# Kernel optimization log

Measured on AMD Instinct MI355X. Metric: run time of the kernel, lower is better.

Reference implementation:

```python
import jax, jax.numpy as jnp
import numpy as np

N = 100000
E = 1600000
F_IN = 512
H1, C1 = 8, 8      # layer-1: 8 heads, 8 dims each (concat -> 64)
H2, C2 = 1, 16     # layer-2: 1 head, num_classes=16
SLOPE = 0.2        # GATConv leaky_relu negative slope


def setup_inputs() -> dict:
    key = jax.random.key(0)
    ks = jax.random.split(key, 10)
    x = jax.random.normal(ks[0], (N, F_IN), dtype=jnp.float32)
    edge_index = jax.random.randint(ks[1], (2, E), 0, N, dtype=jnp.int32)
    s = 0.05
    W1 = jax.random.normal(ks[2], (F_IN, H1 * C1), dtype=jnp.float32) * s
    a1_src = jax.random.normal(ks[3], (H1, C1), dtype=jnp.float32) * s
    a1_dst = jax.random.normal(ks[4], (H1, C1), dtype=jnp.float32) * s
    b1 = jnp.zeros((H1 * C1,), dtype=jnp.float32)
    W2 = jax.random.normal(ks[5], (H1 * C1, H2 * C2), dtype=jnp.float32) * s
    a2_src = jax.random.normal(ks[6], (H2, C2), dtype=jnp.float32) * s
    a2_dst = jax.random.normal(ks[7], (H2, C2), dtype=jnp.float32) * s
    b2 = jnp.zeros((H2 * C2,), dtype=jnp.float32)
    return {"x": x, "edge_index": edge_index, "W1": W1, "a1_src": a1_src,
            "a1_dst": a1_dst, "b1": b1, "W2": W2, "a2_src": a2_src,
            "a2_dst": a2_dst, "b2": b2}


def _gat_conv(h, src, dst, W, a_src, a_dst, b, heads, ch):
    n = h.shape[0]
    hp = (h @ W).reshape(n, heads, ch)                      # [N,H,C]
    al_s = jnp.einsum('nhc,hc->nh', hp, a_src)              # [N,H]
    al_d = jnp.einsum('nhc,hc->nh', hp, a_dst)              # [N,H]
    e = jax.nn.leaky_relu(al_s[src] + al_d[dst], SLOPE)     # [E,H]
    # segment softmax over edges sharing a destination (self-loops guarantee >=1 edge/node)
    emax = jax.lax.stop_gradient(jax.ops.segment_max(e, dst, num_segments=n))
    ee = jnp.exp(e - emax[dst])
    denom = jax.ops.segment_sum(ee, dst, num_segments=n)
    alpha = ee / denom[dst]                                 # [E,H]
    msg = hp[src] * alpha[:, :, None]                       # [E,H,C]
    out = jax.ops.segment_sum(msg, dst, num_segments=n)     # [N,H,C]
    return out.reshape(n, heads * ch) + b


def reference(x, edge_index, W1, a1_src, a1_dst, b1, W2, a2_src, a2_dst, b2):
    n = x.shape[0]
    loops = jnp.arange(n, dtype=edge_index.dtype)           # add_self_loops=True
    src = jnp.concatenate([edge_index[0], loops])
    dst = jnp.concatenate([edge_index[1], loops])
    h = jax.nn.elu(_gat_conv(x, src, dst, W1, a1_src, a1_dst, b1, H1, C1))
    h = _gat_conv(h, src, dst, W2, a2_src, a2_dst, b2, H2, C2)
    return jax.nn.log_softmax(h, axis=1)
```

## Files before the change

### kernel.cpp

```cpp
#include <hip/hip_runtime.h>
#include <hip/hip_bf16.h>

#define N_NODES 100000
#define F_IN    512
#define H1      8
#define C1      8
#define D1      64
#define C2      16
#define SLOPE   0.2f
#define CAP     48
#define PSHIFT  9
#define PPART   196
#define CAPP    9216
#define CHUNK   4096

typedef __bf16 bf16_t;
typedef bf16_t bf16x8 __attribute__((ext_vector_type(8)));
typedef float  f32x4  __attribute__((ext_vector_type(4)));

__global__ __launch_bounds__(256) void wcvt_kernel(
    const float* __restrict__ W, bf16_t* __restrict__ Bt)
{
    int i = blockIdx.x * 256 + threadIdx.x;
    if (i >= 64 * 512) return;
    int nn = i >> 9, k = i & 511;
    Bt[i] = (bf16_t)W[k * 64 + nn];
}

__global__ __launch_bounds__(256) void part_kernel(
    const int* __restrict__ ei, int* __restrict__ pcnt, int2* __restrict__ pfifo,
    int E, int total)
{
    __shared__ int hist[PPART];
    __shared__ int lofs[PPART];
    __shared__ int gbase[PPART];
    __shared__ int cursor[PPART];
    __shared__ int sdata[256];
    __shared__ int2 fifo[CHUNK];

    const int t = threadIdx.x;
    const int chunk0 = (int)blockIdx.x * CHUNK;

    for (int i = t; i < PPART; i += 256) hist[i] = 0;
    __syncthreads();

    int srcs[16], dsts[16];
    const int e0 = chunk0 + t * 16;
    if (e0 + 16 <= E) {
#pragma unroll
        for (int q = 0; q < 4; ++q) {
            int4 s = *(const int4*)(ei + e0 + q * 4);
            int4 d = *(const int4*)(ei + E + e0 + q * 4);
            srcs[q*4+0]=s.x; srcs[q*4+1]=s.y; srcs[q*4+2]=s.z; srcs[q*4+3]=s.w;
            dsts[q*4+0]=d.x; dsts[q*4+1]=d.y; dsts[q*4+2]=d.z; dsts[q*4+3]=d.w;
        }
    } else {
#pragma unroll
        for (int j = 0; j < 16; ++j) {
            int e = e0 + j;
            if (e < E)          { srcs[j] = ei[e]; dsts[j] = ei[E + e]; }
            else if (e < total) { srcs[j] = dsts[j] = e - E; }
            else                { srcs[j] = -1;    dsts[j] = -1; }
        }
    }
#pragma unroll
    for (int j = 0; j < 16; ++j)
        if (dsts[j] >= 0) atomicAdd(&hist[dsts[j] >> PSHIFT], 1);
    __syncthreads();

    int hv = (t < PPART) ? hist[t] : 0;
    sdata[t] = hv;
    __syncthreads();
    for (int off = 1; off < 256; off <<= 1) {
        int x = (t >= off) ? sdata[t - off] : 0;
        __syncthreads();
        sdata[t] += x;
        __syncthreads();
    }
    if (t < PPART) {
        int lo = sdata[t] - hv;
        lofs[t]   = lo;
        cursor[t] = lo;
        gbase[t]  = hv ? atomicAdd(&pcnt[t], hv) : 0;
    }
    __syncthreads();

#pragma unroll
    for (int j = 0; j < 16; ++j) {
        if (dsts[j] >= 0) {
            int p = dsts[j] >> PSHIFT;
            int slot = atomicAdd(&cursor[p], 1);
            fifo[slot] = make_int2(srcs[j], dsts[j]);
        }
    }
    __syncthreads();

    const int w = t >> 6, lane = t & 63;
    for (int p = w; p < PPART; p += 4) {
        int len = hist[p];
        int lo  = lofs[p];
        int gb  = gbase[p];
        int2* dstp = pfifo + (size_t)p * CAPP;
        for (int j = lane; j < len; j += 64) {
            int g = gb + j;
            if (g < CAPP) dstp[g] = fifo[lo + j];
        }
    }
}

__global__ __launch_bounds__(256) void place_kernel(
    const int2* __restrict__ pfifo, const int* __restrict__ pcnt,
    int* __restrict__ buckets, int* __restrict__ cnt, int n)
{
    __shared__ int lcnt[1 << PSHIFT];
    const int p = blockIdx.x;
    const int dbase = p << PSHIFT;
    const int nd = min(1 << PSHIFT, n - dbase);
    const int t = threadIdx.x;
    for (int i = t; i < nd; i += 256) lcnt[i] = 0;
    __syncthreads();

    int len = pcnt[p]; if (len > CAPP) len = CAPP;
    const int2* f = pfifo + (size_t)p * CAPP;

    int i = t;
    for (; i + 768 < len; i += 1024) {
        int2 e0 = f[i], e1 = f[i + 256], e2 = f[i + 512], e3 = f[i + 768];
        int s0 = atomicAdd(&lcnt[e0.y - dbase], 1);
        int s1 = atomicAdd(&lcnt[e1.y - dbase], 1);
        int s2 = atomicAdd(&lcnt[e2.y - dbase], 1);
        int s3 = atomicAdd(&lcnt[e3.y - dbase], 1);
        if (s0 < CAP) buckets[(size_t)e0.y * CAP + s0] = e0.x;
        if (s1 < CAP) buckets[(size_t)e1.y * CAP + s1] = e1.x;
        if (s2 < CAP) buckets[(size_t)e2.y * CAP + s2] = e2.x;
        if (s3 < CAP) buckets[(size_t)e3.y * CAP + s3] = e3.x;
    }
    for (; i < len; i += 256) {
        int2 e = f[i];
        int s = atomicAdd(&lcnt[e.y - dbase], 1);
        if (s < CAP) buckets[(size_t)e.y * CAP + s] = e.x;
    }
    __syncthreads();
    for (int i2 = t; i2 < nd; i2 += 256) cnt[dbase + i2] = min(lcnt[i2], CAP);
}

__global__ __launch_bounds__(256) void gemm1_kernel(
    const float* __restrict__ X, const bf16_t* __restrict__ Bt,
    const float* __restrict__ a1s, const float* __restrict__ a1d,
    bf16_t* __restrict__ HPb, float* __restrict__ als1, float* __restrict__ ald1,
    int n)
{
    __shared__ __align__(16) bf16_t Asm[4096];
    __shared__ __align__(16) bf16_t Bsm[4096];

    const int t = threadIdx.x;
    const int rowbase = (int)blockIdx.x * 64;
    const int wave = t >> 6;
    const int lane = t & 63;

    const int srow  = t >> 2;
    const int skloc = (t & 3) * 16;

    const int grow = rowbase + srow;
    const bool rok = grow < n;
    const float*  xrow = X  + (size_t)grow * F_IN;
    const bf16_t* brow = Bt + (size_t)srow * F_IN;

    int offA[2];
#pragma unroll
    for (int u = 0; u < 2; ++u) {
        int kloc = skloc + u * 8;
        int s    = kloc >> 5;
        int quad = (kloc >> 3) & 3;
        offA[u] = s * 2048 + (((srow >> 4) * 64) + quad * 16 + (srow & 15)) * 8;
    }

    f32x4 acc[4];
#pragma unroll
    for (int nt = 0; nt < 4; ++nt) acc[nt] = (f32x4){0.f, 0.f, 0.f, 0.f};

    for (int k0 = 0; k0 < F_IN; k0 += 64) {
        float4 xa0, xa1, xa2, xa3;
        if (rok) {
            xa0 = *(const float4*)(xrow + k0 + skloc + 0);
            xa1 = *(const float4*)(xrow + k0 + skloc + 4);
            xa2 = *(const float4*)(xrow + k0 + skloc + 8);
            xa3 = *(const float4*)(xrow + k0 + skloc + 12);
        } else {
            xa0 = xa1 = xa2 = xa3 = make_float4(0.f, 0.f, 0.f, 0.f);
        }
        bf16x8 bb0 = *(const bf16x8*)(brow + k0 + skloc);
        bf16x8 bb1 = *(const bf16x8*)(brow + k0 + skloc + 8);

        __syncthreads();

        bf16x8 af0, af1;
        af0[0]=(bf16_t)xa0.x; af0[1]=(bf16_t)xa0.y; af0[2]=(bf16_t)xa0.z; af0[3]=(bf16_t)xa0.w;
        af0[4]=(bf16_t)xa1.x; af0[5]=(bf16_t)xa1.y; af0[6]=(bf16_t)xa1.z; af0[7]=(bf16_t)xa1.w;
        af1[0]=(bf16_t)xa2.x; af1[1]=(bf16_t)xa2.y; af1[2]=(bf16_t)xa2.z; af1[3]=(bf16_t)xa2.w;
        af1[4]=(bf16_t)xa3.x; af1[5]=(bf16_t)xa3.y; af1[6]=(bf16_t)xa3.z; af1[7]=(bf16_t)xa3.w;
        *(bf16x8*)(Asm + offA[0]) = af0;
        *(bf16x8*)(Asm + offA[1]) = af1;
        *(bf16x8*)(Bsm + offA[0]) = bb0;
        *(bf16x8*)(Bsm + offA[1]) = bb1;

        __syncthreads();

#pragma unroll
        for (int s = 0; s < 2; ++s) {
            bf16x8 a = *(const bf16x8*)(Asm + s * 2048 + (wave * 64 + lane) * 8);
#pragma unroll
            for (int nt = 0; nt < 4; ++nt) {
                bf16x8 b = *(const bf16x8*)(Bsm + s * 2048 + (nt * 64 + lane) * 8);
                acc[nt] = __builtin_amdgcn_mfma_f32_16x16x32_bf16(a, b, acc[nt], 0, 0, 0);
            }
        }
    }

    const int colg = lane & 15;
    const int quad = lane >> 4;
    const int b    = colg >> 3;
    float cs[4], cd[4];
#pragma unroll
    for (int nt = 0; nt < 4; ++nt) {
        cs[nt] = a1s[nt * 16 + colg];
        cd[nt] = a1d[nt * 16 + colg];
    }

#pragma unroll
    for (int i = 0; i < 4; ++i) {
        int r = rowbase + wave * 16 + quad * 4 + i;
        bool ok = r < n;
        if (ok) {
            bf16_t* hr = HPb + (size_t)r * D1;
            hr[colg]      = (bf16_t)acc[0][i];
            hr[16 + colg] = (bf16_t)acc[1][i];
            hr[32 + colg] = (bf16_t)acc[2][i];
            hr[48 + colg] = (bf16_t)acc[3][i];
        }
#pragma unroll
        for (int nt = 0; nt < 4; ++nt) {
            float ps = acc[nt][i] * cs[nt];
            float pd = acc[nt][i] * cd[nt];
            ps += __shfl_xor(ps, 1, 64);  pd += __shfl_xor(pd, 1, 64);
            ps += __shfl_xor(ps, 2, 64);  pd += __shfl_xor(pd, 2, 64);
            ps += __shfl_xor(ps, 4, 64);  pd += __shfl_xor(pd, 4, 64);
            if (ok && (colg & 7) == 0) {
                als1[(size_t)r * 8 + 2 * nt + b] = ps;
                ald1[(size_t)r * 8 + 2 * nt + b] = pd;
            }
        }
    }
}

__global__ __launch_bounds__(256) void agg1_kernel(
    const bf16_t* __restrict__ hp1,
    const float* __restrict__ als, const float* __restrict__ ald,
    const int* __restrict__ cnt, const int* __restrict__ buckets,
    const float* __restrict__ b1,
    float* __restrict__ h1, int n)
{
    int node = blockIdx.x * 4 + (threadIdx.x >> 6);
    if (node >= n) return;
    int lane = threadIdx.x & 63;
    int h = lane >> 3;

    int m = cnt[node]; if (m > CAP) m = CAP;
    const int* bp = buckets + (size_t)node * CAP;
    float ad = ald[node * 8 + h];
    float den = 0.f, acc = 0.f;

    int i = 0;
    for (; i + 8 <= m; i += 8) {
        int s0 = bp[i + 0], s1 = bp[i + 1], s2 = bp[i + 2], s3 = bp[i + 3];
        int s4 = bp[i + 4], s5 = bp[i + 5], s6 = bp[i + 6], s7 = bp[i + 7];
        float a0 = als[s0 * 8 + h], a1 = als[s1 * 8 + h];
        float a2 = als[s2 * 8 + h], a3 = als[s3 * 8 + h];
        float a4 = als[s4 * 8 + h], a5 = als[s5 * 8 + h];
        float a6 = als[s6 * 8 + h], a7 = als[s7 * 8 + h];
        float v0 = (float)hp1[(size_t)s0 * D1 + lane];
        float v1 = (float)hp1[(size_t)s1 * D1 + lane];
        float v2 = (float)hp1[(size_t)s2 * D1 + lane];
        float v3 = (float)hp1[(size_t)s3 * D1 + lane];
        float v4 = (float)hp1[(size_t)s4 * D1 + lane];
        float v5 = (float)hp1[(size_t)s5 * D1 + lane];
        float v6 = (float)hp1[(size_t)s6 * D1 + lane];
        float v7 = (float)hp1[(size_t)s7 * D1 + lane];
        float e0 = a0 + ad; e0 = (e0 > 0.f) ? e0 : SLOPE * e0;
        float e1 = a1 + ad; e1 = (e1 > 0.f) ? e1 : SLOPE * e1;
        float e2 = a2 + ad; e2 = (e2 > 0.f) ? e2 : SLOPE * e2;
        float e3 = a3 + ad; e3 = (e3 > 0.f) ? e3 : SLOPE * e3;
        float e4 = a4 + ad; e4 = (e4 > 0.f) ? e4 : SLOPE * e4;
        float e5 = a5 + ad; e5 = (e5 > 0.f) ? e5 : SLOPE * e5;
        float e6 = a6 + ad; e6 = (e6 > 0.f) ? e6 : SLOPE * e6;
        float e7 = a7 + ad; e7 = (e7 > 0.f) ? e7 : SLOPE * e7;
        float w0 = __expf(e0), w1 = __expf(e1), w2 = __expf(e2), w3 = __expf(e3);
        float w4 = __expf(e4), w5 = __expf(e5), w6 = __expf(e6), w7 = __expf(e7);
        den += ((w0 + w1) + (w2 + w3)) + ((w4 + w5) + (w6 + w7));
        acc = fmaf(w0, v0, acc);
        acc = fmaf(w1, v1, acc);
        acc = fmaf(w2, v2, acc);
        acc = fmaf(w3, v3, acc);
        acc = fmaf(w4, v4, acc);
        acc = fmaf(w5, v5, acc);
        acc = fmaf(w6, v6, acc);
        acc = fmaf(w7, v7, acc);
    }
    for (; i < m; ++i) {
        int s = bp[i];
        float e = als[s * 8 + h] + ad;
        e = (e > 0.f) ? e : SLOPE * e;
        float ee = __expf(e);
        den += ee;
        acc = fmaf(ee, (float)hp1[(size_t)s * D1 + lane], acc);
    }
    float v = acc / den + b1[lane];
    v = (v > 0.f) ? v : (__expf(v) - 1.f);
    h1[(size_t)node * D1 + lane] = v;
}

__global__ __launch_bounds__(256) void gemm2_kernel(
    const float* __restrict__ H, const float* __restrict__ W2,
    const float* __restrict__ a2s, const float* __restrict__ a2d,
    bf16_t* __restrict__ HP2b, float* __restrict__ als2, float* __restrict__ ald2,
    int n)
{
    __shared__ float Ws[64 * 16];
    int t = threadIdx.x;
    for (int i = t; i < 1024; i += 256) Ws[i] = W2[i];
    __syncthreads();
    int idx = blockIdx.x * 256 + t;
    int node = idx >> 4, c = idx & 15;
    if (node >= n) return;
    const float* hr = H + (size_t)node * D1;
    float acc = 0.f;
#pragma unroll 8
    for (int k = 0; k < 64; ++k) acc = fmaf(hr[k], Ws[k * 16 + c], acc);
    HP2b[idx] = (bf16_t)acc;

    float rs = acc * a2s[c];
    float rd = acc * a2d[c];
    rs += __shfl_xor(rs, 8, 16);  rd += __shfl_xor(rd, 8, 16);
    rs += __shfl_xor(rs, 4, 16);  rd += __shfl_xor(rd, 4, 16);
    rs += __shfl_xor(rs, 2, 16);  rd += __shfl_xor(rd, 2, 16);
    rs += __shfl_xor(rs, 1, 16);  rd += __shfl_xor(rd, 1, 16);
    if (c == 0) { als2[node] = rs; ald2[node] = rd; }
}

__global__ __launch_bounds__(256) void agg2_kernel(
    const bf16_t* __restrict__ hp2,
    const float* __restrict__ als, const float* __restrict__ ald,
    const int* __restrict__ cnt, const int* __restrict__ buckets,
    const float* __restrict__ b2,
    float* __restrict__ out, int n)
{
    int node = blockIdx.x * 16 + (threadIdx.x >> 4);
    if (node >= n) return;
    int c = threadIdx.x & 15;

    int m0c = cnt[node]; if (m0c > CAP) m0c = CAP;
    const int* bp = buckets + (size_t)node * CAP;
    float ad = ald[node];
    float den = 0.f, acc = 0.f;

    int i = 0;
    for (; i + 8 <= m0c; i += 8) {
        int s0 = bp[i + 0], s1 = bp[i + 1], s2 = bp[i + 2], s3 = bp[i + 3];
        int s4 = bp[i + 4], s5 = bp[i + 5], s6 = bp[i + 6], s7 = bp[i + 7];
        float a0 = als[s0], a1 = als[s1], a2 = als[s2], a3 = als[s3];
        float a4 = als[s4], a5 = als[s5], a6 = als[s6], a7 = als[s7];
        float v0 = (float)hp2[(size_t)s0 * 16 + c];
        float v1 = (float)hp2[(size_t)s1 * 16 + c];
        float v2 = (float)hp2[(size_t)s2 * 16 + c];
        float v3 = (float)hp2[(size_t)s3 * 16 + c];
        float v4 = (float)hp2[(size_t)s4 * 16 + c];
        float v5 = (float)hp2[(size_t)s5 * 16 + c];
        float v6 = (float)hp2[(size_t)s6 * 16 + c];
        float v7 = (float)hp2[(size_t)s7 * 16 + c];
        float e0 = a0 + ad; e0 = (e0 > 0.f) ? e0 : SLOPE * e0;
        float e1 = a1 + ad; e1 = (e1 > 0.f) ? e1 : SLOPE * e1;
        float e2 = a2 + ad; e2 = (e2 > 0.f) ? e2 : SLOPE * e2;
        float e3 = a3 + ad; e3 = (e3 > 0.f) ? e3 : SLOPE * e3;
        float e4 = a4 + ad; e4 = (e4 > 0.f) ? e4 : SLOPE * e4;
        float e5 = a5 + ad; e5 = (e5 > 0.f) ? e5 : SLOPE * e5;
        float e6 = a6 + ad; e6 = (e6 > 0.f) ? e6 : SLOPE * e6;
        float e7 = a7 + ad; e7 = (e7 > 0.f) ? e7 : SLOPE * e7;
        float w0 = __expf(e0), w1 = __expf(e1), w2 = __expf(e2), w3 = __expf(e3);
        float w4 = __expf(e4), w5 = __expf(e5), w6 = __expf(e6), w7 = __expf(e7);
        den += ((w0 + w1) + (w2 + w3)) + ((w4 + w5) + (w6 + w7));
        acc = fmaf(w0, v0, acc);
        acc = fmaf(w1, v1, acc);
        acc = fmaf(w2, v2, acc);
        acc = fmaf(w3, v3, acc);
        acc = fmaf(w4, v4, acc);
        acc = fmaf(w5, v5, acc);
        acc = fmaf(w6, v6, acc);
        acc = fmaf(w7, v7, acc);
    }
    for (; i < m0c; ++i) {
        int s = bp[i];
        float e = als[s] + ad;
        e = (e > 0.f) ? e : SLOPE * e;
        float ee = __expf(e);
        den += ee;
        acc = fmaf(ee, (float)hp2[(size_t)s * 16 + c], acc);
    }
    float v = acc / den + b2[c];

    float m = v;
    m = fmaxf(m, __shfl_xor(m, 8, 16));
    m = fmaxf(m, __shfl_xor(m, 4, 16));
    m = fmaxf(m, __shfl_xor(m, 2, 16));
    m = fmaxf(m, __shfl_xor(m, 1, 16));
    float ex = __expf(v - m);
    float sum = ex;
    sum += __shfl_xor(sum, 8, 16);
    sum += __shfl_xor(sum, 4, 16);
    sum += __shfl_xor(sum, 2, 16);
    sum += __shfl_xor(sum, 1, 16);
    out[(size_t)node * 16 + c] = v - m - __logf(sum);
}

extern "C" void kernel_launch(void* const* d_in, const int* in_sizes, int n_in,
                              void* d_out, int out_size, void* d_ws, size_t ws_size,
                              hipStream_t stream)
{
    const float* x      = (const float*)d_in[0];
    const int*   ei     = (const int*)  d_in[1];
    const float* W1     = (const float*)d_in[2];
    const float* a1_src = (const float*)d_in[3];
    const float* a1_dst = (const float*)d_in[4];
    const float* b1     = (const float*)d_in[5];
    const float* W2     = (const float*)d_in[6];
    const float* a2_src = (const float*)d_in[7];
    const float* a2_dst = (const float*)d_in[8];
    const float* b2     = (const float*)d_in[9];
    float* out = (float*)d_out;

    const int N = in_sizes[0] / F_IN;
    const int E = in_sizes[1] / 2;
    const int TOT = E + N;

    char* base = (char*)d_ws;
    size_t off = 0;
    auto carve = [&](size_t bytes) -> char* {
        char* p = base + off;
        off += (bytes + 255) & ~(size_t)255;
        return p;
    };
    bf16_t* hp1b    = (bf16_t*)carve((size_t)N * D1 * 2);
    float*  h1      = (float*) carve((size_t)N * D1 * 4);
    bf16_t* hp2b    = (bf16_t*)carve((size_t)N * 16 * 2);
    float*  als1    = (float*) carve((size_t)N * 8 * 4);
    float*  ald1    = (float*) carve((size_t)N * 8 * 4);
    float*  als2    = (float*) carve((size_t)N * 4);
    float*  ald2    = (float*) carve((size_t)N * 4);
    int*    cnt     = (int*)   carve((size_t)N * 4);
    int*    pcnt    = (int*)   carve((size_t)PPART * 4);
    int*    buckets = (int*)   carve((size_t)N * CAP * 4);
    bf16_t* W1b     = (bf16_t*)carve((size_t)64 * 512 * 2);
    int2*  pfifo   = (int2*)h1;

    const int Gp = (TOT + CHUNK - 1) / CHUNK;

    hipMemsetAsync(pcnt, 0, (size_t)PPART * 4, stream);

    wcvt_kernel<<<128, 256, 0, stream>>>(W1, W1b);
    part_kernel<<<Gp, 256, 0, stream>>>(ei, pcnt, pfifo, E, TOT);
    place_kernel<<<PPART, 256, 0, stream>>>(pfifo, pcnt, buckets, cnt, N);

    gemm1_kernel<<<(N + 63) / 64, 256, 0, stream>>>(x, W1b, a1_src, a1_dst,
                                                    hp1b, als1, ald1, N);

    agg1_kernel<<<(N + 3) / 4, 256, 0, stream>>>(hp1b, als1, ald1, cnt, buckets, b1, h1, N);

    gemm2_kernel<<<(N * 16 + 255) / 256, 256, 0, stream>>>(h1, W2, a2_src, a2_dst, hp2b, als2, ald2, N);

    agg2_kernel<<<(N + 15) / 16, 256, 0, stream>>>(hp2b, als2, ald2, cnt, buckets, b2, out, N);
}
```

Before: 515.9 us.

## Load X directly into MFMA registers and stage W1 in LDS by halves

The layer-1 GEMM no longer stages the X tile through shared memory. Each lane loads its A fragment straight from global memory in fp32 and converts it to bf16 in registers. The bf16 weight matrix is staged into LDS once per half of K, in MFMA fragment order. Blocks grow to 512 threads covering 128 rows. This removes the per-k-step LDS writes and barriers for A and should improve how well the X read, the dominant memory stream, is overlapped with the MFMAs. The cost is less coalesced per-lane global reads (16 rows by 32 bytes per wave instruction) and more register pressure.

```diff
diff --git a/kernel.cpp b/kernel.cpp
--- a/kernel.cpp
+++ b/kernel.cpp
@@ -144,77 +144,58 @@
     for (int i2 = t; i2 < nd; i2 += 256) cnt[dbase + i2] = min(lcnt[i2], CAP);
 }
 
-__global__ __launch_bounds__(256) void gemm1_kernel(
+__global__ __launch_bounds__(512, 4) void gemm1_kernel(
     const float* __restrict__ X, const bf16_t* __restrict__ Bt,
     const float* __restrict__ a1s, const float* __restrict__ a1d,
     bf16_t* __restrict__ HPb, float* __restrict__ als1, float* __restrict__ ald1,
     int n)
 {
-    __shared__ __align__(16) bf16_t Asm[4096];
-    __shared__ __align__(16) bf16_t Bsm[4096];
+    __shared__ __align__(16) bf16_t Bsm[8 * 4 * 64 * 8];
 
     const int t = threadIdx.x;
-    const int rowbase = (int)blockIdx.x * 64;
-    const int wave = t >> 6;
+    const int rowbase = (int)blockIdx.x * 128;
+    const int w = t >> 6;
     const int lane = t & 63;
 
-    const int srow  = t >> 2;
-    const int skloc = (t & 3) * 16;
-
-    const int grow = rowbase + srow;
-    const bool rok = grow < n;
-    const float*  xrow = X  + (size_t)grow * F_IN;
-    const bf16_t* brow = Bt + (size_t)srow * F_IN;
-
-    int offA[2];
-#pragma unroll
-    for (int u = 0; u < 2; ++u) {
-        int kloc = skloc + u * 8;
-        int s    = kloc >> 5;
-        int quad = (kloc >> 3) & 3;
-        offA[u] = s * 2048 + (((srow >> 4) * 64) + quad * 16 + (srow & 15)) * 8;
-    }
+    const int rloc = lane & 15;
+    const int koff = (lane >> 4) * 8;
+
+    int grow = rowbase + w * 16 + rloc;
+    int growc = (grow < n) ? grow : (n - 1);
+    const float* arow = X + (size_t)growc * F_IN + koff;
 
     f32x4 acc[4];
 #pragma unroll
     for (int nt = 0; nt < 4; ++nt) acc[nt] = (f32x4){0.f, 0.f, 0.f, 0.f};
 
-    for (int k0 = 0; k0 < F_IN; k0 += 64) {
-        float4 xa0, xa1, xa2, xa3;
-        if (rok) {
-            xa0 = *(const float4*)(xrow + k0 + skloc + 0);
-            xa1 = *(const float4*)(xrow + k0 + skloc + 4);
-            xa2 = *(const float4*)(xrow + k0 + skloc + 8);
-            xa3 = *(const float4*)(xrow + k0 + skloc + 12);
-        } else {
-            xa0 = xa1 = xa2 = xa3 = make_float4(0.f, 0.f, 0.f, 0.f);
-        }
-        bf16x8 bb0 = *(const bf16x8*)(brow + k0 + skloc);
-        bf16x8 bb1 = *(const bf16x8*)(brow + k0 + skloc + 8);
-
+#pragma unroll
+    for (int half = 0; half < 2; ++half) {
+        for (int i = t; i < 2048; i += 512) {
+            int l9 = i & 63;
+            int nt = (i >> 6) & 3;
+            int ks = i >> 8;
+            int row = nt * 16 + (l9 & 15);
+            int col = (half * 8 + ks) * 32 + (l9 >> 4) * 8;
+            *(bf16x8*)(Bsm + (size_t)i * 8) =
+                *(const bf16x8*)(Bt + (size_t)row * F_IN + col);
+        }
         __syncthreads();
 
-        bf16x8 af0, af1;
-        af0[0]=(bf16_t)xa0.x; af0[1]=(bf16_t)xa0.y; af0[2]=(bf16_t)xa0.z; af0[3]=(bf16_t)xa0.w;
-        af0[4]=(bf16_t)xa1.x; af0[5]=(bf16_t)xa1.y; af0[6]=(bf16_t)xa1.z; af0[7]=(bf16_t)xa1.w;
-        af1[0]=(bf16_t)xa2.x; af1[1]=(bf16_t)xa2.y; af1[2]=(bf16_t)xa2.z; af1[3]=(bf16_t)xa2.w;
-        af1[4]=(bf16_t)xa3.x; af1[5]=(bf16_t)xa3.y; af1[6]=(bf16_t)xa3.z; af1[7]=(bf16_t)xa3.w;
-        *(bf16x8*)(Asm + offA[0]) = af0;
-        *(bf16x8*)(Asm + offA[1]) = af1;
-        *(bf16x8*)(Bsm + offA[0]) = bb0;
-        *(bf16x8*)(Bsm + offA[1]) = bb1;
-
+#pragma unroll 4
+        for (int ks = 0; ks < 8; ++ks) {
+            int kg = (half * 8 + ks) * 32;
+            float4 xa0 = *(const float4*)(arow + kg);
+            float4 xa1 = *(const float4*)(arow + kg + 4);
+            bf16x8 af;
+            af[0]=(bf16_t)xa0.x; af[1]=(bf16_t)xa0.y; af[2]=(bf16_t)xa0.z; af[3]=(bf16_t)xa0.w;
+            af[4]=(bf16_t)xa1.x; af[5]=(bf16_t)xa1.y; af[6]=(bf16_t)xa1.z; af[7]=(bf16_t)xa1.w;
+#pragma unroll
+            for (int nt = 0; nt < 4; ++nt) {
+                bf16x8 b = *(const bf16x8*)(Bsm + ((ks * 4 + nt) * 64 + lane) * 8);
+                acc[nt] = __builtin_amdgcn_mfma_f32_16x16x32_bf16(af, b, acc[nt], 0, 0, 0);
+            }
+        }
         __syncthreads();
-
-#pragma unroll
-        for (int s = 0; s < 2; ++s) {
-            bf16x8 a = *(const bf16x8*)(Asm + s * 2048 + (wave * 64 + lane) * 8);
-#pragma unroll
-            for (int nt = 0; nt < 4; ++nt) {
-                bf16x8 b = *(const bf16x8*)(Bsm + s * 2048 + (nt * 64 + lane) * 8);
-                acc[nt] = __builtin_amdgcn_mfma_f32_16x16x32_bf16(a, b, acc[nt], 0, 0, 0);
-            }
-        }
     }
 
     const int colg = lane & 15;
@@ -229,7 +210,7 @@
 
 #pragma unroll
     for (int i = 0; i < 4; ++i) {
-        int r = rowbase + wave * 16 + quad * 4 + i;
+        int r = rowbase + w * 16 + quad * 4 + i;
         bool ok = r < n;
         if (ok) {
             bf16_t* hr = HPb + (size_t)r * D1;
@@ -469,8 +450,8 @@
     part_kernel<<<Gp, 256, 0, stream>>>(ei, pcnt, pfifo, E, TOT);
     place_kernel<<<PPART, 256, 0, stream>>>(pfifo, pcnt, buckets, cnt, N);
 
-    gemm1_kernel<<<(N + 63) / 64, 256, 0, stream>>>(x, W1b, a1_src, a1_dst,
-                                                    hp1b, als1, ald1, N);
+    gemm1_kernel<<<(N + 127) / 128, 512, 0, stream>>>(x, W1b, a1_src, a1_dst,
+                                                      hp1b, als1, ald1, N);
 
     agg1_kernel<<<(N + 3) / 4, 256, 0, stream>>>(hp1b, als1, ald1, cnt, buckets, b1, h1, N);
 
```

After: 507.4 us. About the same (-1.7%).
